# Optimization experiments

Measured on AMD Instinct MI355X. Metric: run time of the kernel, lower is better.

## Reference

```python
import math
import jax, jax.numpy as jnp
import numpy as np

FILTER_ORDER = 64
FILTER_EMB_DIM = 5
HIDDEN = 256
SHIFT = 0.05
FAST_DECAY_PCT = 0.3
SLOW_DECAY_PCT = 1.5
TARGET = 0.01


def setup_inputs() -> dict:
    key = jax.random.key(0)
    ks = jax.random.split(key, 8)
    B, C, L = 8, HIDDEN, 8192

    def lin_w(k, fan_out, fan_in):
        return jax.random.normal(k, (fan_out, fan_in), jnp.float32) / np.sqrt(fan_in).astype(np.float32)

    return {
        "x": jax.random.normal(ks[0], (B, C, L), jnp.float32),
        "W1": lin_w(ks[1], FILTER_ORDER, FILTER_EMB_DIM),
        "b1": jnp.zeros((FILTER_ORDER,), jnp.float32),
        "freq0": jnp.ones((1, FILTER_ORDER), jnp.float32),
        "W2": lin_w(ks[2], FILTER_ORDER, FILTER_ORDER),
        "b2": jnp.zeros((FILTER_ORDER,), jnp.float32),
        "freq1": jnp.ones((1, FILTER_ORDER), jnp.float32),
        "W3": lin_w(ks[3], FILTER_ORDER, FILTER_ORDER),
        "b3": jnp.zeros((FILTER_ORDER,), jnp.float32),
        "freq2": jnp.ones((1, FILTER_ORDER), jnp.float32),
        "Wout": lin_w(ks[4], HIDDEN, FILTER_ORDER),
        "D": jax.random.normal(ks[5], (HIDDEN,), jnp.float32),
        "L": L,
    }


def _pos_emb(L):
    # HyenaDnaPositionalEmbedding: z (1, L, emb_dim), t (1, L, 1)
    t = jnp.linspace(0.0, 1.0, L, dtype=jnp.float32)[None, :, None]
    t_rescaled = jnp.linspace(0.0, L - 1, L, dtype=jnp.float32)[None, :, None]
    w = 2.0 * math.pi * t_rescaled / L  # (1, L, 1)
    bands = (FILTER_EMB_DIM - 1) // 2
    f = jnp.linspace(1e-4, bands - 1, bands, dtype=jnp.float32)[None, None]  # (1, 1, bands)
    z = jnp.concatenate([t, jnp.cos(-f * w), jnp.sin(-f * w)], axis=-1)  # (1, L, emb_dim)
    return z, t


def _filter_kernel(W1, b1, freq0, W2, b2, freq1, W3, b3, freq2, Wout, L):
    z, t = _pos_emb(L)
    h = jnp.sin(freq0 * (jnp.einsum('ble,oe->blo', z, W1) + b1))
    h = jnp.sin(freq1 * (jnp.einsum('blo,po->blp', h, W2) + b2))
    h = jnp.sin(freq2 * (jnp.einsum('blo,po->blp', h, W3) + b3))
    h = jnp.einsum('blo,do->bld', h, Wout)  # (1, L, HIDDEN)
    # exponential modulation window
    max_decay = math.log(TARGET) / FAST_DECAY_PCT
    min_decay = math.log(TARGET) / SLOW_DECAY_PCT
    deltas = jnp.linspace(min_decay, max_decay, HIDDEN, dtype=jnp.float32)[None, None]
    decay = jnp.exp(-t * jnp.abs(deltas))  # (1, L, HIDDEN)
    h = h * (decay + SHIFT)
    return h[0].T  # (HIDDEN, L) channels-major kernel


def _fftconv(u, k, D):
    # y = conv(u, k) + u * D via FFT, zero-padded to 2L (linear convolution)
    L = u.shape[-1]
    fft_size = 2 * L
    k_f = jnp.fft.rfft(k.astype(jnp.float32), n=fft_size) / fft_size  # (C, fft_size//2+1)
    u_f = jnp.fft.rfft(u.astype(jnp.float32), n=fft_size)             # (B, C, fft_size//2+1)
    y = jnp.fft.irfft(u_f * k_f, n=fft_size, norm='forward')[..., :L]
    return (y + u * D[:, None]).astype(u.dtype)


def reference(x, W1, b1, freq0, W2, b2, freq1, W3, b3, freq2, Wout, D, L):
    k = _filter_kernel(W1, b1, freq0, W2, b2, freq1, W3, b3, freq2, Wout, L)
    return _fftconv(x, k, D)
```

## Files before the change

### kernel.cpp

```cpp
#include <hip/hip_runtime.h>

#define L_SEQ 8192
#define NTH 512
#define HID 256
#define PIDX(i) ((i) + ((i) >> 4))
#define LDS_SZ 8704

#define ANG16 3.83495196971410315e-4f
#define ANG8  7.66990393942820630e-4f
#define CS16 0.99999992646571789f
#define SN16 3.83495187571395563e-4f
#define CS8  0.99999970586287223f
#define SN8  7.66990318742704490e-4f
#define C707 0.70710678118654752f

__device__ float2 TWID[4088];
template<int M> struct TWOFF;
template<> struct TWOFF<512> { static constexpr int v = 0;    };
template<> struct TWOFF<64>  { static constexpr int v = 3584; };
template<> struct TWOFF<8>   { static constexpr int v = 4032; };

__global__ void twid_kernel() {
  int i = threadIdx.x;
  #pragma unroll
  for (int j = 1; j <= 7; ++j) {
    float s, c;
    sincosf(-6.2831853071795864769f * (float)(i*j) / 4096.0f, &s, &c);
    TWID[i*7 + j-1] = make_float2(c, s);
  }
  if (i < 64) {
    #pragma unroll
    for (int j = 1; j <= 7; ++j) {
      float s, c;
      sincosf(-6.2831853071795864769f * (float)(i*j) / 512.0f, &s, &c);
      TWID[3584 + i*7 + j-1] = make_float2(c, s);
    }
  }
  if (i < 8) {
    #pragma unroll
    for (int j = 1; j <= 7; ++j) {
      float s, c;
      sincosf(-6.2831853071795864769f * (float)(i*j) / 64.0f, &s, &c);
      TWID[4032 + i*7 + j-1] = make_float2(c, s);
    }
  }
}

__device__ __forceinline__ float2 cmul(float2 a, float2 b) {
  return make_float2(a.x*b.x - a.y*b.y, a.x*b.y + a.y*b.x);
}
__device__ __forceinline__ float2 cadd(float2 a, float2 b){ return make_float2(a.x+b.x, a.y+b.y); }
__device__ __forceinline__ float2 csub(float2 a, float2 b){ return make_float2(a.x-b.x, a.y-b.y); }

__device__ __forceinline__ void bf4_fwd(float2 a0, float2 a1, float2 a2, float2 a3,
                                        float2& o0, float2& o1, float2& o2, float2& o3) {
  float2 t0 = cadd(a0,a2), t1 = csub(a0,a2), t2 = cadd(a1,a3), t3 = csub(a1,a3);
  o0 = cadd(t0,t2);
  o2 = csub(t0,t2);
  o1 = make_float2(t1.x + t3.y, t1.y - t3.x);
  o3 = make_float2(t1.x - t3.y, t1.y + t3.x);
}
__device__ __forceinline__ void bf4_inv(float2 c0, float2 c1, float2 c2, float2 c3,
                                        float2& o0, float2& o1, float2& o2, float2& o3) {
  float2 u0 = cadd(c0,c2), u2 = csub(c0,c2), u1 = cadd(c1,c3);
  float2 v3 = make_float2(c3.y - c1.y, c1.x - c3.x);
  o0 = cadd(u0,u1); o2 = csub(u0,u1); o1 = cadd(u2,v3); o3 = csub(u2,v3);
}

__device__ __forceinline__ void fwd8(float2 P[8]) {
  float2 e0=cadd(P[0],P[4]), e1=cadd(P[1],P[5]), e2=cadd(P[2],P[6]), e3=cadd(P[3],P[7]);
  float2 o0=csub(P[0],P[4]), o1=csub(P[1],P[5]), o2=csub(P[2],P[6]), o3=csub(P[3],P[7]);
  o1 = make_float2((o1.x+o1.y)*C707, (o1.y-o1.x)*C707);
  o2 = make_float2(o2.y, -o2.x);
  o3 = make_float2((o3.y-o3.x)*C707, -(o3.x+o3.y)*C707);
  float2 q0,q1,q2,q3;
  bf4_fwd(e0,e1,e2,e3,q0,q1,q2,q3);
  P[0]=q0; P[2]=q1; P[4]=q2; P[6]=q3;
  bf4_fwd(o0,o1,o2,o3,q0,q1,q2,q3);
  P[1]=q0; P[3]=q1; P[5]=q2; P[7]=q3;
}
__device__ __forceinline__ void inv8(float2 P[8]) {
  float2 E0,E1,E2,E3,O0,O1,O2,O3;
  bf4_inv(P[0],P[2],P[4],P[6],E0,E1,E2,E3);
  bf4_inv(P[1],P[3],P[5],P[7],O0,O1,O2,O3);
  O1 = make_float2((O1.x-O1.y)*C707, (O1.x+O1.y)*C707);
  O2 = make_float2(-O2.y, O2.x);
  O3 = make_float2(-(O3.x+O3.y)*C707, (O3.x-O3.y)*C707);
  P[0]=cadd(E0,O0); P[4]=csub(E0,O0);
  P[1]=cadd(E1,O1); P[5]=csub(E1,O1);
  P[2]=cadd(E2,O2); P[6]=csub(E2,O2);
  P[3]=cadd(E3,O3); P[7]=csub(E3,O3);
}

template<int M>
__device__ __forceinline__ void fwd_stage8(float2* __restrict__ X, int t) {
  #pragma unroll
  for (int r = 0; r < 2; ++r) {
    int s = t + NTH*r;
    int i2 = s & (M-1);
    int g  = s / M;
    int base = g*8*M + i2;
    const float2* __restrict__ w = TWID + TWOFF<M>::v + i2*7;
    float2 P[8];
    #pragma unroll
    for (int j=0;j<8;++j) P[j] = X[PIDX(base + j*M)];
    fwd8(P);
    X[PIDX(base)] = P[0];
    #pragma unroll
    for (int j=1;j<8;++j) X[PIDX(base + j*M)] = cmul(P[j], w[j-1]);
  }
}
template<int M>
__device__ __forceinline__ void inv_stage8(float2* __restrict__ X, int t) {
  #pragma unroll
  for (int r = 0; r < 2; ++r) {
    int s = t + NTH*r;
    int i2 = s & (M-1);
    int g  = s / M;
    int base = g*8*M + i2;
    const float2* __restrict__ w = TWID + TWOFF<M>::v + i2*7;
    float2 P[8];
    P[0] = X[PIDX(base)];
    #pragma unroll
    for (int j=1;j<8;++j) {
      float2 wj = w[j-1];
      P[j] = cmul(X[PIDX(base + j*M)], make_float2(wj.x, -wj.y));
    }
    inv8(P);
    #pragma unroll
    for (int j=0;j<8;++j) X[PIDX(base + j*M)] = P[j];
  }
}

__device__ __forceinline__ void fft_mid_fwd(float2* __restrict__ X, int t) {
  __syncthreads();
  fwd_stage8<512>(X,t); __syncthreads();
  fwd_stage8<64>(X,t);  __syncthreads();
  fwd_stage8<8>(X,t);   __syncthreads();
}
__device__ __forceinline__ void fft_mid_inv(float2* __restrict__ X, int t) {
  __syncthreads();
  inv_stage8<8>(X,t);   __syncthreads();
  inv_stage8<64>(X,t);  __syncthreads();
  inv_stage8<512>(X,t); __syncthreads();
}

__device__ __forceinline__ void middle_pointwise(float2* __restrict__ X,
                                                 const float2* __restrict__ K, int t) {
  #pragma unroll
  for (int r = 0; r < 2; ++r) {
    int base = 8*(t + NTH*r);
    float2 kreg[8];
    #pragma unroll
    for (int q=0;q<8;++q) kreg[q] = K[base+q];
    float2 P[8];
    #pragma unroll
    for (int q=0;q<8;++q) P[q] = X[PIDX(base+q)];
    fwd8(P);
    #pragma unroll
    for (int q=0;q<8;++q) P[q] = cmul(P[q], kreg[q]);
    inv8(P);
    #pragma unroll
    for (int q=0;q<8;++q) X[PIDX(base+q)] = P[q];
  }
}

__global__ __launch_bounds__(256) void mlp_kernel(
    const float* __restrict__ W1, const float* __restrict__ b1, const float* __restrict__ fq0,
    const float* __restrict__ W2, const float* __restrict__ b2, const float* __restrict__ fq1,
    const float* __restrict__ W3, const float* __restrict__ b3, const float* __restrict__ fq2,
    float* __restrict__ h3g) {
  __shared__ float hs[2][16][64];
  int tid = threadIdx.x;
  int lane = tid & 63, w = tid >> 6;
  int l0 = blockIdx.x * 16;

  float w1r[5];
  #pragma unroll
  for (int e = 0; e < 5; ++e) w1r[e] = W1[lane*5+e];
  float b1v = b1[lane], f0 = fq0[lane];
  #pragma unroll
  for (int r = 0; r < 4; ++r) {
    int l = l0 + w + 4*r;
    float t = (float)l * (1.0f / (float)(L_SEQ - 1));
    float ang = 6.2831853071795864769f * (float)l / (float)L_SEQ;
    float s0, c0, s1, c1;
    __sincosf(1e-4f * ang, &s0, &c0);
    __sincosf(ang, &s1, &c1);
    float acc = b1v + t*w1r[0] + c0*w1r[1] + c1*w1r[2] - s0*w1r[3] - s1*w1r[4];
    hs[0][w + 4*r][lane] = __sinf(f0 * acc);
  }
  __syncthreads();

  float wr[64];
  #pragma unroll
  for (int j = 0; j < 16; ++j) *(float4*)&wr[4*j] = *(const float4*)&W2[lane*64 + 4*j];
  float b2v = b2[lane], f1 = fq1[lane];
  #pragma unroll
  for (int r = 0; r < 4; ++r) {
    int ll = w + 4*r;
    float a0 = 0.f, a1 = 0.f, a2 = 0.f, a3 = 0.f;
    #pragma unroll
    for (int o = 0; o < 64; o += 4) {
      a0 += hs[0][ll][o+0] * wr[o+0];
      a1 += hs[0][ll][o+1] * wr[o+1];
      a2 += hs[0][ll][o+2] * wr[o+2];
      a3 += hs[0][ll][o+3] * wr[o+3];
    }
    hs[1][ll][lane] = __sinf(f1 * (b2v + ((a0+a1)+(a2+a3))));
  }
  __syncthreads();

  #pragma unroll
  for (int j = 0; j < 16; ++j) *(float4*)&wr[4*j] = *(const float4*)&W3[lane*64 + 4*j];
  float b3v = b3[lane], f2 = fq2[lane];
  #pragma unroll
  for (int r = 0; r < 4; ++r) {
    int ll = w + 4*r;
    float a0 = 0.f, a1 = 0.f, a2 = 0.f, a3 = 0.f;
    #pragma unroll
    for (int o = 0; o < 64; o += 4) {
      a0 += hs[1][ll][o+0] * wr[o+0];
      a1 += hs[1][ll][o+1] * wr[o+1];
      a2 += hs[1][ll][o+2] * wr[o+2];
      a3 += hs[1][ll][o+3] * wr[o+3];
    }
    h3g[(size_t)(l0 + ll) * 64 + lane] = __sinf(f2 * (b3v + ((a0+a1)+(a2+a3))));
  }
}

__global__ __launch_bounds__(256) void kwrite_kernel(const float* __restrict__ h3g,
                                                     const float* __restrict__ Wout,
                                                     const float* __restrict__ Dv,
                                                     float* __restrict__ kbuf) {
  __shared__ float tileh[256][65];
  int tid = threadIdx.x;
  int l0 = blockIdx.x * 256;
  int c0 = blockIdx.y * 32;
  {
    const float4* src = (const float4*)(h3g + (size_t)l0 * 64);
    #pragma unroll
    for (int q = 0; q < 16; ++q) {
      int idx = tid + 256*q;
      int row = idx >> 4, col4 = idx & 15;
      float4 v = src[idx];
      tileh[row][col4*4+0] = v.x;
      tileh[row][col4*4+1] = v.y;
      tileh[row][col4*4+2] = v.z;
      tileh[row][col4*4+3] = v.w;
    }
  }
  __syncthreads();
  float hr[64];
  #pragma unroll
  for (int o = 0; o < 64; ++o) hr[o] = tileh[tid][o];
  int l = l0 + tid;
  float t = (float)l * (1.0f / (float)(L_SEQ - 1));
  const float mind = -3.0701134573253945f;
  const float maxd = -15.350567286626972f;
  for (int jj = 0; jj < 32; ++jj) {
    int c = c0 + jj;
    float a0 = 0.f, a1 = 0.f, a2 = 0.f, a3 = 0.f;
    #pragma unroll
    for (int o = 0; o < 64; o += 4) {
      a0 += hr[o+0] * Wout[c*64+o+0];
      a1 += hr[o+1] * Wout[c*64+o+1];
      a2 += hr[o+2] * Wout[c*64+o+2];
      a3 += hr[o+3] * Wout[c*64+o+3];
    }
    float acc = (a0+a1)+(a2+a3);
    float delta = mind + (maxd - mind) * ((float)c * (1.0f/255.0f));
    float dec = __expf(-t * fabsf(delta)) + 0.05f;
    float v = acc * dec;
    if (l == 0) v += Dv[c];
    kbuf[(size_t)c * L_SEQ + l] = v;
  }
}

__global__ __launch_bounds__(NTH) void kf_kernel(const float* __restrict__ kbuf,
                                                 float2* __restrict__ Kf) {
  __shared__ float2 X[LDS_SZ];
  int pipe = blockIdx.x;
  int c = blockIdx.y;
  int t = threadIdx.x;
  const float* kr = kbuf + (size_t)c * L_SEQ;
  const float sc = 1.0f / 16384.0f;
  #pragma unroll
  for (int r = 0; r < 2; ++r) {
    int n0 = 4*t + 2048*r;
    float4 lo4 = *(const float4*)(kr + n0);
    float4 hi4 = *(const float4*)(kr + n0 + 4096);
    if (pipe == 0) {
      float sb, cb; __sincosf(-ANG8 * (float)n0, &sb, &cb);
      float2 w8 = make_float2(cb, sb);
      #pragma unroll
      for (int j = 0; j < 4; ++j) {
        if (j) w8 = cmul(w8, make_float2(CS8, -SN8));
        float klo = ((const float*)&lo4)[j];
        float khi = ((const float*)&hi4)[j];
        X[PIDX(n0+j)]      = make_float2(klo + khi, 0.f);
        float d = klo - khi;
        X[PIDX(n0+j+4096)] = make_float2(d * w8.x, d * w8.y);
      }
    } else {
      float sb, cb; __sincosf(-ANG16 * (float)n0, &sb, &cb);
      float2 w16 = make_float2(cb, sb);
      #pragma unroll
      for (int j = 0; j < 4; ++j) {
        if (j) w16 = cmul(w16, make_float2(CS16, -SN16));
        float klo = ((const float*)&lo4)[j];
        float khi = ((const float*)&hi4)[j];
        float2 vlo = make_float2(klo * w16.x, klo * w16.y);
        float2 vhi = make_float2(khi * w16.y, -khi * w16.x);
        float2 w8 = cmul(w16, w16);
        X[PIDX(n0+j)]      = cadd(vlo, vhi);
        X[PIDX(n0+j+4096)] = cmul(csub(vlo, vhi), w8);
      }
    }
  }
  fft_mid_fwd(X, t);
  #pragma unroll
  for (int r = 0; r < 2; ++r) {
    int base = 8*(t + NTH*r);
    float2 P[8];
    #pragma unroll
    for (int q=0;q<8;++q) P[q] = X[PIDX(base+q)];
    fwd8(P);
    float2* out = Kf + (size_t)c * 16384 + pipe*8192 + base;
    #pragma unroll
    for (int q=0;q<8;++q) out[q] = make_float2(P[q].x*sc, P[q].y*sc);
  }
}

__global__ __launch_bounds__(NTH) void conv_kernel(const float* __restrict__ x,
                                                   const float2* __restrict__ Kf,
                                                   float* __restrict__ y) {
  __shared__ float2 X[LDS_SZ];
  int c = blockIdx.x;
  int p = blockIdx.y;
  int t = threadIdx.x;
  const float* u0 = x + ((size_t)p       * HID + c) * L_SEQ;
  const float* u1 = x + ((size_t)(p + 4) * HID + c) * L_SEQ;
  const float2* KA = Kf + (size_t)c * 16384;
  const float2* KB = KA + 8192;
  float* y0 = y + ((size_t)p       * HID + c) * L_SEQ;
  float* y1 = y + ((size_t)(p + 4) * HID + c) * L_SEQ;

  #pragma unroll
  for (int r = 0; r < 2; ++r) {
    int n0 = 4*t + 2048*r;
    float4 a0 = *(const float4*)(u0 + n0);
    float4 a1 = *(const float4*)(u1 + n0);
    float4 b0 = *(const float4*)(u0 + n0 + 4096);
    float4 b1 = *(const float4*)(u1 + n0 + 4096);
    float sb, cb; __sincosf(-ANG16 * (float)n0, &sb, &cb);
    float2 w16 = make_float2(cb, sb);
    #pragma unroll
    for (int j = 0; j < 4; ++j) {
      if (j) w16 = cmul(w16, make_float2(CS16, -SN16));
      float2 vlo = cmul(make_float2(((const float*)&a0)[j], ((const float*)&a1)[j]), w16);
      float2 vhi = cmul(make_float2(((const float*)&b0)[j], ((const float*)&b1)[j]),
                        make_float2(w16.y, -w16.x));
      float2 w8 = cmul(w16, w16);
      X[PIDX(n0+j)]      = cadd(vlo, vhi);
      X[PIDX(n0+j+4096)] = cmul(csub(vlo, vhi), w8);
    }
  }
  fft_mid_fwd(X, t);
  middle_pointwise(X, KB, t);
  fft_mid_inv(X, t);
  float2 stash[16];
  #pragma unroll
  for (int r = 0; r < 2; ++r) {
    int n0 = 4*t + 2048*r;
    float sb, cb; __sincosf(ANG16 * (float)n0, &sb, &cb);
    float2 w16b = make_float2(cb, sb);
    #pragma unroll
    for (int j = 0; j < 4; ++j) {
      if (j) w16b = cmul(w16b, make_float2(CS16, SN16));
      float2 P = X[PIDX(n0+j)], Q = X[PIDX(n0+j+4096)];
      float2 w8b = cmul(w16b, w16b);
      float2 tt = cmul(Q, w8b);
      stash[r*4+j]     = cmul(cadd(P, tt), w16b);
      stash[8 + r*4+j] = cmul(csub(P, tt), make_float2(-w16b.y, w16b.x));
    }
  }
  __syncthreads();

  #pragma unroll
  for (int r = 0; r < 2; ++r) {
    int n0 = 4*t + 2048*r;
    float4 a0 = *(const float4*)(u0 + n0);
    float4 a1 = *(const float4*)(u1 + n0);
    float4 b0 = *(const float4*)(u0 + n0 + 4096);
    float4 b1 = *(const float4*)(u1 + n0 + 4096);
    float sb, cb; __sincosf(-ANG8 * (float)n0, &sb, &cb);
    float2 w8 = make_float2(cb, sb);
    #pragma unroll
    for (int j = 0; j < 4; ++j) {
      if (j) w8 = cmul(w8, make_float2(CS8, -SN8));
      float2 vlo = make_float2(((const float*)&a0)[j], ((const float*)&a1)[j]);
      float2 vhi = make_float2(((const float*)&b0)[j], ((const float*)&b1)[j]);
      X[PIDX(n0+j)]      = cadd(vlo, vhi);
      X[PIDX(n0+j+4096)] = cmul(csub(vlo, vhi), w8);
    }
  }
  fft_mid_fwd(X, t);
  middle_pointwise(X, KA, t);
  fft_mid_inv(X, t);
  #pragma unroll
  for (int r = 0; r < 2; ++r) {
    int n0 = 4*t + 2048*r;
    float sb, cb; __sincosf(ANG8 * (float)n0, &sb, &cb);
    float2 w8b = make_float2(cb, sb);
    float4 w00, w01, w10, w11;
    #pragma unroll
    for (int j = 0; j < 4; ++j) {
      if (j) w8b = cmul(w8b, make_float2(CS8, SN8));
      float2 P = X[PIDX(n0+j)], Q = X[PIDX(n0+j+4096)];
      float2 tt = cmul(Q, w8b);
      float2 lo = cadd(cadd(P, tt), stash[r*4+j]);
      float2 hi = cadd(csub(P, tt), stash[8 + r*4+j]);
      ((float*)&w00)[j] = lo.x; ((float*)&w01)[j] = lo.y;
      ((float*)&w10)[j] = hi.x; ((float*)&w11)[j] = hi.y;
    }
    *(float4*)(y0 + n0)        = w00;
    *(float4*)(y1 + n0)        = w01;
    *(float4*)(y0 + n0 + 4096) = w10;
    *(float4*)(y1 + n0 + 4096) = w11;
  }
}

extern "C" void kernel_launch(void* const* d_in, const int* in_sizes, int n_in,
                              void* d_out, int out_size, void* d_ws, size_t ws_size,
                              hipStream_t stream) {
  const float* x    = (const float*)d_in[0];
  const float* W1   = (const float*)d_in[1];
  const float* b1   = (const float*)d_in[2];
  const float* fq0  = (const float*)d_in[3];
  const float* W2   = (const float*)d_in[4];
  const float* b2   = (const float*)d_in[5];
  const float* fq1  = (const float*)d_in[6];
  const float* W3   = (const float*)d_in[7];
  const float* b3   = (const float*)d_in[8];
  const float* fq2  = (const float*)d_in[9];
  const float* Wout = (const float*)d_in[10];
  const float* Dv   = (const float*)d_in[11];

  float*  kbuf = (float*)d_ws;
  float2* Kf   = (float2*)((char*)d_ws + (size_t)HID * L_SEQ * sizeof(float));
  float*  h3g  = (float*)((char*)d_ws + 38ull*1024*1024);
  float*  y    = (float*)d_out;

  twid_kernel  <<<dim3(1),     512, 0, stream>>>();
  mlp_kernel   <<<dim3(512),   256, 0, stream>>>(W1,b1,fq0,W2,b2,fq1,W3,b3,fq2,h3g);
  kwrite_kernel<<<dim3(32, 8), 256, 0, stream>>>(h3g, Wout, Dv, kbuf);
  kf_kernel    <<<dim3(2, 256), NTH, 0, stream>>>(kbuf, Kf);
  conv_kernel  <<<dim3(256, 4), NTH, 0, stream>>>(x, Kf, y);
}
```

Baseline: 164.9 us.

## Process two FFT signals per block to share twiddles and kernel spectra

Each block of the conv and kernel-FFT stages now handles two independent FFTs in two LDS buffers, so twiddle loads, kernel-spectrum loads and barriers are amortized across twice the work. The conv grid halves from 1024 to 512 blocks, each covering four batches instead of two, and kf_kernel merges its two pipes into one block per channel. This doubles LDS use to about 139 KB per block and raises register pressure from the 16-entry stash arrays, which limits residency to one block per CU and halves the block count for latency hiding.

Measured after the change: 164.7 us. About the same (-0.1%).

```diff
diff --git a/kernel.cpp b/kernel.cpp
--- a/kernel.cpp
+++ b/kernel.cpp
@@ -93,75 +93,94 @@
 }
 
 template<int M>
-__device__ __forceinline__ void fwd_stage8(float2* __restrict__ X, int t) {
+__device__ __forceinline__ void fwd_stage8_2(float2* __restrict__ X0,
+                                             float2* __restrict__ X1, int t) {
   #pragma unroll
   for (int r = 0; r < 2; ++r) {
     int s = t + NTH*r;
     int i2 = s & (M-1);
     int g  = s / M;
     int base = g*8*M + i2;
-    const float2* __restrict__ w = TWID + TWOFF<M>::v + i2*7;
-    float2 P[8];
-    #pragma unroll
-    for (int j=0;j<8;++j) P[j] = X[PIDX(base + j*M)];
-    fwd8(P);
-    X[PIDX(base)] = P[0];
-    #pragma unroll
-    for (int j=1;j<8;++j) X[PIDX(base + j*M)] = cmul(P[j], w[j-1]);
+    const float2* __restrict__ wp = TWID + TWOFF<M>::v + i2*7;
+    float2 w[7];
+    #pragma unroll
+    for (int j=0;j<7;++j) w[j] = wp[j];
+    float2 Pa[8], Pb[8];
+    #pragma unroll
+    for (int j=0;j<8;++j) { Pa[j] = X0[PIDX(base + j*M)]; Pb[j] = X1[PIDX(base + j*M)]; }
+    fwd8(Pa); fwd8(Pb);
+    X0[PIDX(base)] = Pa[0];
+    X1[PIDX(base)] = Pb[0];
+    #pragma unroll
+    for (int j=1;j<8;++j) {
+      X0[PIDX(base + j*M)] = cmul(Pa[j], w[j-1]);
+      X1[PIDX(base + j*M)] = cmul(Pb[j], w[j-1]);
+    }
   }
 }
 template<int M>
-__device__ __forceinline__ void inv_stage8(float2* __restrict__ X, int t) {
+__device__ __forceinline__ void inv_stage8_2(float2* __restrict__ X0,
+                                             float2* __restrict__ X1, int t) {
   #pragma unroll
   for (int r = 0; r < 2; ++r) {
     int s = t + NTH*r;
     int i2 = s & (M-1);
     int g  = s / M;
     int base = g*8*M + i2;
-    const float2* __restrict__ w = TWID + TWOFF<M>::v + i2*7;
-    float2 P[8];
-    P[0] = X[PIDX(base)];
+    const float2* __restrict__ wp = TWID + TWOFF<M>::v + i2*7;
+    float2 w[7];
+    #pragma unroll
+    for (int j=0;j<7;++j) { float2 v = wp[j]; w[j] = make_float2(v.x, -v.y); }
+    float2 Pa[8], Pb[8];
+    Pa[0] = X0[PIDX(base)];
+    Pb[0] = X1[PIDX(base)];
     #pragma unroll
     for (int j=1;j<8;++j) {
-      float2 wj = w[j-1];
-      P[j] = cmul(X[PIDX(base + j*M)], make_float2(wj.x, -wj.y));
-    }
-    inv8(P);
-    #pragma unroll
-    for (int j=0;j<8;++j) X[PIDX(base + j*M)] = P[j];
-  }
-}
-
-__device__ __forceinline__ void fft_mid_fwd(float2* __restrict__ X, int t) {
+      Pa[j] = cmul(X0[PIDX(base + j*M)], w[j-1]);
+      Pb[j] = cmul(X1[PIDX(base + j*M)], w[j-1]);
+    }
+    inv8(Pa); inv8(Pb);
+    #pragma unroll
+    for (int j=0;j<8;++j) {
+      X0[PIDX(base + j*M)] = Pa[j];
+      X1[PIDX(base + j*M)] = Pb[j];
+    }
+  }
+}
+
+__device__ __forceinline__ void fft_mid_fwd2(float2* __restrict__ X0,
+                                             float2* __restrict__ X1, int t) {
   __syncthreads();
-  fwd_stage8<512>(X,t); __syncthreads();
-  fwd_stage8<64>(X,t);  __syncthreads();
-  fwd_stage8<8>(X,t);   __syncthreads();
-}
-__device__ __forceinline__ void fft_mid_inv(float2* __restrict__ X, int t) {
+  fwd_stage8_2<512>(X0,X1,t); __syncthreads();
+  fwd_stage8_2<64>(X0,X1,t);  __syncthreads();
+  fwd_stage8_2<8>(X0,X1,t);   __syncthreads();
+}
+__device__ __forceinline__ void fft_mid_inv2(float2* __restrict__ X0,
+                                             float2* __restrict__ X1, int t) {
   __syncthreads();
-  inv_stage8<8>(X,t);   __syncthreads();
-  inv_stage8<64>(X,t);  __syncthreads();
-  inv_stage8<512>(X,t); __syncthreads();
-}
-
-__device__ __forceinline__ void middle_pointwise(float2* __restrict__ X,
-                                                 const float2* __restrict__ K, int t) {
+  inv_stage8_2<8>(X0,X1,t);   __syncthreads();
+  inv_stage8_2<64>(X0,X1,t);  __syncthreads();
+  inv_stage8_2<512>(X0,X1,t); __syncthreads();
+}
+
+__device__ __forceinline__ void middle_pointwise2(float2* __restrict__ X0,
+                                                  float2* __restrict__ X1,
+                                                  const float2* __restrict__ K, int t) {
   #pragma unroll
   for (int r = 0; r < 2; ++r) {
     int base = 8*(t + NTH*r);
     float2 kreg[8];
     #pragma unroll
     for (int q=0;q<8;++q) kreg[q] = K[base+q];
-    float2 P[8];
-    #pragma unroll
-    for (int q=0;q<8;++q) P[q] = X[PIDX(base+q)];
-    fwd8(P);
-    #pragma unroll
-    for (int q=0;q<8;++q) P[q] = cmul(P[q], kreg[q]);
-    inv8(P);
-    #pragma unroll
-    for (int q=0;q<8;++q) X[PIDX(base+q)] = P[q];
+    float2 Pa[8], Pb[8];
+    #pragma unroll
+    for (int q=0;q<8;++q) { Pa[q] = X0[PIDX(base+q)]; Pb[q] = X1[PIDX(base+q)]; }
+    fwd8(Pa); fwd8(Pb);
+    #pragma unroll
+    for (int q=0;q<8;++q) { Pa[q] = cmul(Pa[q], kreg[q]); Pb[q] = cmul(Pb[q], kreg[q]); }
+    inv8(Pa); inv8(Pb);
+    #pragma unroll
+    for (int q=0;q<8;++q) { X0[PIDX(base+q)] = Pa[q]; X1[PIDX(base+q)] = Pb[q]; }
   }
 }
 
@@ -279,9 +298,9 @@
 
 __global__ __launch_bounds__(NTH) void kf_kernel(const float* __restrict__ kbuf,
                                                  float2* __restrict__ Kf) {
-  __shared__ float2 X[LDS_SZ];
-  int pipe = blockIdx.x;
-  int c = blockIdx.y;
+  __shared__ float2 X0[LDS_SZ];
+  __shared__ float2 X1[LDS_SZ];
+  int c = blockIdx.x;
   int t = threadIdx.x;
   const float* kr = kbuf + (size_t)c * L_SEQ;
   const float sc = 1.0f / 16384.0f;
@@ -290,86 +309,98 @@
     int n0 = 4*t + 2048*r;
     float4 lo4 = *(const float4*)(kr + n0);
     float4 hi4 = *(const float4*)(kr + n0 + 4096);
-    if (pipe == 0) {
-      float sb, cb; __sincosf(-ANG8 * (float)n0, &sb, &cb);
-      float2 w8 = make_float2(cb, sb);
-      #pragma unroll
-      for (int j = 0; j < 4; ++j) {
-        if (j) w8 = cmul(w8, make_float2(CS8, -SN8));
-        float klo = ((const float*)&lo4)[j];
-        float khi = ((const float*)&hi4)[j];
-        X[PIDX(n0+j)]      = make_float2(klo + khi, 0.f);
-        float d = klo - khi;
-        X[PIDX(n0+j+4096)] = make_float2(d * w8.x, d * w8.y);
-      }
-    } else {
-      float sb, cb; __sincosf(-ANG16 * (float)n0, &sb, &cb);
-      float2 w16 = make_float2(cb, sb);
-      #pragma unroll
-      for (int j = 0; j < 4; ++j) {
-        if (j) w16 = cmul(w16, make_float2(CS16, -SN16));
-        float klo = ((const float*)&lo4)[j];
-        float khi = ((const float*)&hi4)[j];
-        float2 vlo = make_float2(klo * w16.x, klo * w16.y);
-        float2 vhi = make_float2(khi * w16.y, -khi * w16.x);
-        float2 w8 = cmul(w16, w16);
-        X[PIDX(n0+j)]      = cadd(vlo, vhi);
-        X[PIDX(n0+j+4096)] = cmul(csub(vlo, vhi), w8);
-      }
-    }
-  }
-  fft_mid_fwd(X, t);
+    float s8, c8;  __sincosf(-ANG8  * (float)n0, &s8, &c8);
+    float s16, c16; __sincosf(-ANG16 * (float)n0, &s16, &c16);
+    float2 w8  = make_float2(c8, s8);
+    float2 w16 = make_float2(c16, s16);
+    #pragma unroll
+    for (int j = 0; j < 4; ++j) {
+      if (j) { w8 = cmul(w8, make_float2(CS8, -SN8)); w16 = cmul(w16, make_float2(CS16, -SN16)); }
+      float klo = ((const float*)&lo4)[j];
+      float khi = ((const float*)&hi4)[j];
+      X0[PIDX(n0+j)]      = make_float2(klo + khi, 0.f);
+      float d = klo - khi;
+      X0[PIDX(n0+j+4096)] = make_float2(d * w8.x, d * w8.y);
+      float2 vlo = make_float2(klo * w16.x, klo * w16.y);
+      float2 vhi = make_float2(khi * w16.y, -khi * w16.x);
+      float2 w8x = cmul(w16, w16);
+      X1[PIDX(n0+j)]      = cadd(vlo, vhi);
+      X1[PIDX(n0+j+4096)] = cmul(csub(vlo, vhi), w8x);
+    }
+  }
+  fft_mid_fwd2(X0, X1, t);
   #pragma unroll
   for (int r = 0; r < 2; ++r) {
     int base = 8*(t + NTH*r);
-    float2 P[8];
-    #pragma unroll
-    for (int q=0;q<8;++q) P[q] = X[PIDX(base+q)];
-    fwd8(P);
-    float2* out = Kf + (size_t)c * 16384 + pipe*8192 + base;
-    #pragma unroll
-    for (int q=0;q<8;++q) out[q] = make_float2(P[q].x*sc, P[q].y*sc);
+    float2 P0[8], P1[8];
+    #pragma unroll
+    for (int q=0;q<8;++q) { P0[q] = X0[PIDX(base+q)]; P1[q] = X1[PIDX(base+q)]; }
+    fwd8(P0); fwd8(P1);
+    float2* out0 = Kf + (size_t)c * 16384 + base;
+    float2* out1 = out0 + 8192;
+    #pragma unroll
+    for (int q=0;q<8;++q) {
+      out0[q] = make_float2(P0[q].x*sc, P0[q].y*sc);
+      out1[q] = make_float2(P1[q].x*sc, P1[q].y*sc);
+    }
   }
 }
 
 __global__ __launch_bounds__(NTH) void conv_kernel(const float* __restrict__ x,
                                                    const float2* __restrict__ Kf,
                                                    float* __restrict__ y) {
-  __shared__ float2 X[LDS_SZ];
+  __shared__ float2 X0[LDS_SZ];
+  __shared__ float2 X1[LDS_SZ];
   int c = blockIdx.x;
   int p = blockIdx.y;
   int t = threadIdx.x;
-  const float* u0 = x + ((size_t)p       * HID + c) * L_SEQ;
-  const float* u1 = x + ((size_t)(p + 4) * HID + c) * L_SEQ;
+  const float* u00 = x + ((size_t)(p)     * HID + c) * L_SEQ;
+  const float* u01 = x + ((size_t)(p + 4) * HID + c) * L_SEQ;
+  const float* u10 = x + ((size_t)(p + 2) * HID + c) * L_SEQ;
+  const float* u11 = x + ((size_t)(p + 6) * HID + c) * L_SEQ;
   const float2* KA = Kf + (size_t)c * 16384;
   const float2* KB = KA + 8192;
-  float* y0 = y + ((size_t)p       * HID + c) * L_SEQ;
-  float* y1 = y + ((size_t)(p + 4) * HID + c) * L_SEQ;
+  float* y00 = y + ((size_t)(p)     * HID + c) * L_SEQ;
+  float* y01 = y + ((size_t)(p + 4) * HID + c) * L_SEQ;
+  float* y10 = y + ((size_t)(p + 2) * HID + c) * L_SEQ;
+  float* y11 = y + ((size_t)(p + 6) * HID + c) * L_SEQ;
 
   #pragma unroll
   for (int r = 0; r < 2; ++r) {
     int n0 = 4*t + 2048*r;
-    float4 a0 = *(const float4*)(u0 + n0);
-    float4 a1 = *(const float4*)(u1 + n0);
-    float4 b0 = *(const float4*)(u0 + n0 + 4096);
-    float4 b1 = *(const float4*)(u1 + n0 + 4096);
+    float4 a00 = *(const float4*)(u00 + n0);
+    float4 a01 = *(const float4*)(u01 + n0);
+    float4 b00 = *(const float4*)(u00 + n0 + 4096);
+    float4 b01 = *(const float4*)(u01 + n0 + 4096);
+    float4 a10 = *(const float4*)(u10 + n0);
+    float4 a11 = *(const float4*)(u11 + n0);
+    float4 b10 = *(const float4*)(u10 + n0 + 4096);
+    float4 b11 = *(const float4*)(u11 + n0 + 4096);
     float sb, cb; __sincosf(-ANG16 * (float)n0, &sb, &cb);
     float2 w16 = make_float2(cb, sb);
     #pragma unroll
     for (int j = 0; j < 4; ++j) {
       if (j) w16 = cmul(w16, make_float2(CS16, -SN16));
-      float2 vlo = cmul(make_float2(((const float*)&a0)[j], ((const float*)&a1)[j]), w16);
-      float2 vhi = cmul(make_float2(((const float*)&b0)[j], ((const float*)&b1)[j]),
-                        make_float2(w16.y, -w16.x));
+      float2 wmi = make_float2(w16.y, -w16.x);
       float2 w8 = cmul(w16, w16);
-      X[PIDX(n0+j)]      = cadd(vlo, vhi);
-      X[PIDX(n0+j+4096)] = cmul(csub(vlo, vhi), w8);
-    }
-  }
-  fft_mid_fwd(X, t);
-  middle_pointwise(X, KB, t);
-  fft_mid_inv(X, t);
-  float2 stash[16];
+      {
+        float2 vlo = cmul(make_float2(((const float*)&a00)[j], ((const float*)&a01)[j]), w16);
+        float2 vhi = cmul(make_float2(((const float*)&b00)[j], ((const float*)&b01)[j]), wmi);
+        X0[PIDX(n0+j)]      = cadd(vlo, vhi);
+        X0[PIDX(n0+j+4096)] = cmul(csub(vlo, vhi), w8);
+      }
+      {
+        float2 vlo = cmul(make_float2(((const float*)&a10)[j], ((const float*)&a11)[j]), w16);
+        float2 vhi = cmul(make_float2(((const float*)&b10)[j], ((const float*)&b11)[j]), wmi);
+        X1[PIDX(n0+j)]      = cadd(vlo, vhi);
+        X1[PIDX(n0+j+4096)] = cmul(csub(vlo, vhi), w8);
+      }
+    }
+  }
+  fft_mid_fwd2(X0, X1, t);
+  middle_pointwise2(X0, X1, KB, t);
+  fft_mid_inv2(X0, X1, t);
+  float2 st0[16], st1[16];
   #pragma unroll
   for (int r = 0; r < 2; ++r) {
     int n0 = 4*t + 2048*r;
@@ -378,11 +409,20 @@
     #pragma unroll
     for (int j = 0; j < 4; ++j) {
       if (j) w16b = cmul(w16b, make_float2(CS16, SN16));
-      float2 P = X[PIDX(n0+j)], Q = X[PIDX(n0+j+4096)];
       float2 w8b = cmul(w16b, w16b);
-      float2 tt = cmul(Q, w8b);
-      stash[r*4+j]     = cmul(cadd(P, tt), w16b);
-      stash[8 + r*4+j] = cmul(csub(P, tt), make_float2(-w16b.y, w16b.x));
+      float2 wib = make_float2(-w16b.y, w16b.x);
+      {
+        float2 P = X0[PIDX(n0+j)], Q = X0[PIDX(n0+j+4096)];
+        float2 tt = cmul(Q, w8b);
+        st0[r*4+j]     = cmul(cadd(P, tt), w16b);
+        st0[8 + r*4+j] = cmul(csub(P, tt), wib);
+      }
+      {
+        float2 P = X1[PIDX(n0+j)], Q = X1[PIDX(n0+j+4096)];
+        float2 tt = cmul(Q, w8b);
+        st1[r*4+j]     = cmul(cadd(P, tt), w16b);
+        st1[8 + r*4+j] = cmul(csub(P, tt), wib);
+      }
     }
   }
   __syncthreads();
@@ -390,44 +430,77 @@
   #pragma unroll
   for (int r = 0; r < 2; ++r) {
     int n0 = 4*t + 2048*r;
-    float4 a0 = *(const float4*)(u0 + n0);
-    float4 a1 = *(const float4*)(u1 + n0);
-    float4 b0 = *(const float4*)(u0 + n0 + 4096);
-    float4 b1 = *(const float4*)(u1 + n0 + 4096);
+    float4 a00 = *(const float4*)(u00 + n0);
+    float4 a01 = *(const float4*)(u01 + n0);
+    float4 b00 = *(const float4*)(u00 + n0 + 4096);
+    float4 b01 = *(const float4*)(u01 + n0 + 4096);
+    float4 a10 = *(const float4*)(u10 + n0);
+    float4 a11 = *(const float4*)(u11 + n0);
+    float4 b10 = *(const float4*)(u10 + n0 + 4096);
+    float4 b11 = *(const float4*)(u11 + n0 + 4096);
     float sb, cb; __sincosf(-ANG8 * (float)n0, &sb, &cb);
     float2 w8 = make_float2(cb, sb);
     #pragma unroll
     for (int j = 0; j < 4; ++j) {
       if (j) w8 = cmul(w8, make_float2(CS8, -SN8));
-      float2 vlo = make_float2(((const float*)&a0)[j], ((const float*)&a1)[j]);
-      float2 vhi = make_float2(((const float*)&b0)[j], ((const float*)&b1)[j]);
-      X[PIDX(n0+j)]      = cadd(vlo, vhi);
-      X[PIDX(n0+j+4096)] = cmul(csub(vlo, vhi), w8);
-    }
-  }
-  fft_mid_fwd(X, t);
-  middle_pointwise(X, KA, t);
-  fft_mid_inv(X, t);
+      {
+        float2 vlo = make_float2(((const float*)&a00)[j], ((const float*)&a01)[j]);
+        float2 vhi = make_float2(((const float*)&b00)[j], ((const float*)&b01)[j]);
+        X0[PIDX(n0+j)]      = cadd(vlo, vhi);
+        X0[PIDX(n0+j+4096)] = cmul(csub(vlo, vhi), w8);
+      }
+      {
+        float2 vlo = make_float2(((const float*)&a10)[j], ((const float*)&a11)[j]);
+        float2 vhi = make_float2(((const float*)&b10)[j], ((const float*)&b11)[j]);
+        X1[PIDX(n0+j)]      = cadd(vlo, vhi);
+        X1[PIDX(n0+j+4096)] = cmul(csub(vlo, vhi), w8);
+      }
+    }
+  }
+  fft_mid_fwd2(X0, X1, t);
+  middle_pointwise2(X0, X1, KA, t);
+  fft_mid_inv2(X0, X1, t);
   #pragma unroll
   for (int r = 0; r < 2; ++r) {
     int n0 = 4*t + 2048*r;
     float sb, cb; __sincosf(ANG8 * (float)n0, &sb, &cb);
-    float2 w8b = make_float2(cb, sb);
-    float4 w00, w01, w10, w11;
-    #pragma unroll
-    for (int j = 0; j < 4; ++j) {
-      if (j) w8b = cmul(w8b, make_float2(CS8, SN8));
-      float2 P = X[PIDX(n0+j)], Q = X[PIDX(n0+j+4096)];
-      float2 tt = cmul(Q, w8b);
-      float2 lo = cadd(cadd(P, tt), stash[r*4+j]);
-      float2 hi = cadd(csub(P, tt), stash[8 + r*4+j]);
-      ((float*)&w00)[j] = lo.x; ((float*)&w01)[j] = lo.y;
-      ((float*)&w10)[j] = hi.x; ((float*)&w11)[j] = hi.y;
-    }
-    *(float4*)(y0 + n0)        = w00;
-    *(float4*)(y1 + n0)        = w01;
-    *(float4*)(y0 + n0 + 4096) = w10;
-    *(float4*)(y1 + n0 + 4096) = w11;
+    float2 w8b0 = make_float2(cb, sb);
+    {
+      float2 w8b = w8b0;
+      float4 w00, w01, w10, w11;
+      #pragma unroll
+      for (int j = 0; j < 4; ++j) {
+        if (j) w8b = cmul(w8b, make_float2(CS8, SN8));
+        float2 P = X0[PIDX(n0+j)], Q = X0[PIDX(n0+j+4096)];
+        float2 tt = cmul(Q, w8b);
+        float2 lo = cadd(cadd(P, tt), st0[r*4+j]);
+        float2 hi = cadd(csub(P, tt), st0[8 + r*4+j]);
+        ((float*)&w00)[j] = lo.x; ((float*)&w01)[j] = lo.y;
+        ((float*)&w10)[j] = hi.x; ((float*)&w11)[j] = hi.y;
+      }
+      *(float4*)(y00 + n0)        = w00;
+      *(float4*)(y01 + n0)        = w01;
+      *(float4*)(y00 + n0 + 4096) = w10;
+      *(float4*)(y01 + n0 + 4096) = w11;
+    }
+    {
+      float2 w8b = w8b0;
+      float4 w00, w01, w10, w11;
+      #pragma unroll
+      for (int j = 0; j < 4; ++j) {
+        if (j) w8b = cmul(w8b, make_float2(CS8, SN8));
+        float2 P = X1[PIDX(n0+j)], Q = X1[PIDX(n0+j+4096)];
+        float2 tt = cmul(Q, w8b);
+        float2 lo = cadd(cadd(P, tt), st1[r*4+j]);
+        float2 hi = cadd(csub(P, tt), st1[8 + r*4+j]);
+        ((float*)&w00)[j] = lo.x; ((float*)&w01)[j] = lo.y;
+        ((float*)&w10)[j] = hi.x; ((float*)&w11)[j] = hi.y;
+      }
+      *(float4*)(y10 + n0)        = w00;
+      *(float4*)(y11 + n0)        = w01;
+      *(float4*)(y10 + n0 + 4096) = w10;
+      *(float4*)(y11 + n0 + 4096) = w11;
+    }
   }
 }
 
@@ -455,6 +528,6 @@
   twid_kernel  <<<dim3(1),     512, 0, stream>>>();
   mlp_kernel   <<<dim3(512),   256, 0, stream>>>(W1,b1,fq0,W2,b2,fq1,W3,b3,fq2,h3g);
   kwrite_kernel<<<dim3(32, 8), 256, 0, stream>>>(h3g, Wout, Dv, kbuf);
-  kf_kernel    <<<dim3(2, 256), NTH, 0, stream>>>(kbuf, Kf);
-  conv_kernel  <<<dim3(256, 4), NTH, 0, stream>>>(x, Kf, y);
-}
+  kf_kernel    <<<dim3(256),    NTH, 0, stream>>>(kbuf, Kf);
+  conv_kernel  <<<dim3(256, 2), NTH, 0, stream>>>(x, Kf, y);
+}
```
